# Optimization experiments

Hardware: AMD Instinct MI355X
Metric: run time of the kernel (lower is better)

Reference implementation:

```python
import jax, jax.numpy as jnp
import numpy as np

B, L, N, C = 128, 12, 307, 4
HID = 64
PRE = 3
BN_EPS = 1e-5


def _hamilton(w):
    # w: (in_features//4, out_features) -> hamilton: (in_features, out_features)
    r, i, j, k = jnp.split(w, 4, axis=1)
    return jnp.concatenate([
        jnp.concatenate([r, -i, -j, -k], axis=0),
        jnp.concatenate([i, r, -k, j], axis=0),
        jnp.concatenate([j, k, r, -i], axis=0),
        jnp.concatenate([k, -j, i, r], axis=0),
    ], axis=1)


def setup_inputs() -> dict:
    key = jax.random.key(0)
    ks = jax.random.split(key, 14)

    def u(k, shape, s):
        return jax.random.uniform(k, shape, dtype=jnp.float32, minval=-s, maxval=s)

    history_data = jax.random.uniform(ks[0], (B, L, N, C), dtype=jnp.float32)
    adj = jax.random.uniform(ks[1], (N, N), dtype=jnp.float32)
    # QGNN layer weights (space='q'): layer0 (C//4, HID), layer1 (HID//4, HID)
    w0 = u(ks[2], (C // 4, HID), (6.0 / (C // 4 + HID)) ** 0.5)
    w1 = u(ks[3], (HID // 4, HID), (6.0 / (HID // 4 + HID)) ** 0.5)
    # BatchNorm1d (eval-mode) params for the 2 layers
    bn_gamma = jnp.ones((2, HID), jnp.float32)
    bn_beta = jnp.zeros((2, HID), jnp.float32)
    bn_mean = jnp.zeros((2, HID), jnp.float32)
    bn_var = jnp.ones((2, HID), jnp.float32)
    tid_emb = jax.random.normal(ks[4], (288, 5), dtype=jnp.float32)
    dw_emb = jax.random.normal(ks[5], (7, 5), dtype=jnp.float32)
    gin = HID + 11
    sg = (1.0 / HID) ** 0.5
    w_ih = u(ks[6], (3 * HID, gin), sg)
    w_hh = u(ks[7], (3 * HID, HID), sg)
    b_ih = u(ks[8], (3 * HID,), sg)
    b_hh = u(ks[9], (3 * HID,), sg)
    fc_w = u(ks[10], (1, HID), sg)
    fc_b = u(ks[11], (1,), sg)
    return dict(history_data=history_data, adj=adj, w0=w0, w1=w1,
                bn_gamma=bn_gamma, bn_beta=bn_beta, bn_mean=bn_mean, bn_var=bn_var,
                tid_emb=tid_emb, dw_emb=dw_emb,
                w_ih=w_ih, w_hh=w_hh, b_ih=b_ih, b_hh=b_hh,
                fc_w=fc_w, fc_b=fc_b)


def reference(history_data, adj, w0, w1, bn_gamma, bn_beta, bn_mean, bn_var,
              tid_emb, dw_emb, w_ih, w_hh, b_ih, b_hh, fc_w, fc_b):
    b, l, n, c = history_data.shape
    hist = jnp.transpose(history_data, (0, 2, 1, 3))  # (B, N, L, C)
    speed = hist[..., :1]
    tid = jnp.round(hist[..., 1] * 287).astype(jnp.int32)
    dw = jnp.round(hist[..., 2] * 6).astype(jnp.int32)
    T_D = tid_emb[tid]  # (B, N, L, 5)
    D_W = dw_emb[dw]    # (B, N, L, 5)

    # symmetric adjacency normalization: D^{-1/2} (A + I) D^{-1/2}
    a = adj + jnp.eye(n, dtype=adj.dtype)
    dinv = jnp.sum(a, axis=1) ** -0.5
    a_n = dinv[:, None] * a * dinv[None, :]

    # QGNN layers, vectorized over all timesteps (same weights every t; dropout=identity in eval)
    x = hist
    for i, w in enumerate([w0, w1]):
        ham = _hamilton(w)
        support = jnp.einsum('bnlc,cd->bnld', x, ham)
        out = jnp.einsum('nm,bmld->bnld', a_n, support)
        scale = bn_gamma[i] / jnp.sqrt(bn_var[i] + BN_EPS)
        out = (out - bn_mean[i]) * scale + bn_beta[i]
        x = jnp.tanh(out)

    feat = jnp.concatenate([x, speed, T_D, D_W], axis=-1)  # (B, N, L, HID+11)
    seq = feat.reshape(b * n, l, -1).transpose(1, 0, 2)     # (L, B*N, HID+11)

    hid = w_hh.shape[1]

    def gru_step(h, xt):
        gi = xt @ w_ih.T + b_ih
        gh = h @ w_hh.T + b_hh
        ir, iz, inn = jnp.split(gi, 3, axis=-1)
        hr, hz, hn = jnp.split(gh, 3, axis=-1)
        r = jax.nn.sigmoid(ir + hr)
        z = jax.nn.sigmoid(iz + hz)
        ncand = jnp.tanh(inn + r * hn)
        h_new = (1.0 - z) * ncand + z * h
        return h_new, h_new

    h0 = jnp.zeros((b * n, hid), feat.dtype)
    _, hs = jax.lax.scan(gru_step, h0, seq)        # (L, B*N, HID)
    hs = hs.transpose(1, 0, 2).reshape(b, n, l, hid)
    out = jax.nn.relu(hs[:, :, -PRE:, :])
    out = out @ fc_w.T + fc_b                       # (B, N, PRE, 1)
    return jnp.transpose(out, (0, 2, 1, 3))         # (B, PRE, N, 1)
```

## Files before the change

kernel.cpp:

```cpp
#include <hip/hip_runtime.h>
#include <hip/hip_fp16.h>


#define NND 307
#define BBATCH 128
#define LSEQ 12
#define HIDN 64
#define JTOT (BBATCH*LSEQ*HIDN)
#define NROWS (NND*BBATCH)
#define KPAD 320
#define MSTR 312
#define F2S 80

#define OFF_DINV  0
#define OFF_HAM0  320
#define OFF_HAM1  576
#define OFF_WIHP  4672
#define OFF_WHHP  12352
#define OFF_ANG   18496
#define OFF_S1T   69696
#define OFF_S0T   15405120
#define OFF_FEATH 15405120

typedef _Float16 half8 __attribute__((ext_vector_type(8)));
typedef float f32x4 __attribute__((ext_vector_type(4)));

__global__ void k_dinv(const float* __restrict__ adj, float* __restrict__ dinv){
  int n = blockIdx.x; int lane = threadIdx.x;
  float s = 0.f;
  for (int m = lane; m < NND; m += 64) s += adj[n*NND+m] + (m==n ? 1.f : 0.f);
  #pragma unroll
  for (int o = 32; o > 0; o >>= 1) s += __shfl_down(s, o);
  if (lane == 0) dinv[n] = 1.f/sqrtf(s);
}

__global__ void k_anG(const float* __restrict__ adj, const float* __restrict__ dinv,
                      __half* __restrict__ anG){
  int id = blockIdx.x*256 + threadIdx.x;
  if (id >= KPAD*KPAD) return;
  int n = id / KPAD, m = id % KPAD;
  float v = 0.f;
  if (n < NND && m < NND)
    v = dinv[n] * (adj[n*NND+m] + (n==m ? 1.f : 0.f)) * dinv[m];
  int ks = m >> 5, g = (m >> 3) & 3, j = m & 7;
  anG[(((ks*4 + g)*320 + n) << 3) + j] = __float2half(v);
}

__global__ void k_ham(const float* __restrict__ w0, const float* __restrict__ w1,
                      float* __restrict__ ham0T, float* __restrict__ ham1){
  const int  comp[4][4] = {{0,1,2,3},{1,0,3,2},{2,3,0,1},{3,2,1,0}};
  const float sgn[4][4] = {{1.f,1.f,1.f,1.f},{-1.f,1.f,1.f,-1.f},
                           {-1.f,-1.f,1.f,1.f},{-1.f,1.f,-1.f,1.f}};
  int id = blockIdx.x*256 + threadIdx.x;
  if (id < 64) {
    int d = id, qb = d>>4, cc = d&15;
    #pragma unroll
    for (int c = 0; c < 4; ++c)
      ham0T[d*4+c] = sgn[c][qb] * w0[comp[c][qb]*16 + cc];
  }
  int id1 = id - 256;
  if (id1 >= 0 && id1 < 4096) {
    int drow = id1 >> 6, d = id1 & 63;
    int pb = drow>>4, rr = drow&15, qb = d>>4, cc = d&15;
    ham1[id1] = sgn[pb][qb] * w1[rr*64 + comp[pb][qb]*16 + cc];
  }
}

__global__ void k_wT(const float* __restrict__ w_ih, const float* __restrict__ w_hh,
                     __half* __restrict__ wihP, __half* __restrict__ whhP){
  int id = blockIdx.x*256 + threadIdx.x;
  if (id < 10*192*8) {
    int j = id & 7, col = (id >> 3) % 192, g = id / (192*8);
    int k = g*8 + j;
    wihP[id] = __float2half(k < 75 ? w_ih[col*75 + k] : 0.f);
  } else {
    int id2 = id - 10*192*8;
    if (id2 < 8*192*8) {
      int j = id2 & 7, col = (id2 >> 3) % 192, g = id2 / (192*8);
      whhP[id2] = __float2half(w_hh[col*64 + g*8 + j]);
    }
  }
}

__global__ __launch_bounds__(256) void k_s0(const float* __restrict__ hist,
                                            const float* __restrict__ ham0Tg,
                                            __half* __restrict__ S0T){
  __shared__ float4 histL[320];
  const int t = threadIdx.x;
  const int bl = blockIdx.x;
  for (int k = t; k < 320; k += 256)
    histL[k] = (k < NND) ? *(const float4*)(hist + ((size_t)bl*NND + k)*4)
                         : make_float4(0.f,0.f,0.f,0.f);
  __syncthreads();
  if (t < 154) {
    const int k0 = 2*t;
    const float4 hA = histL[k0], hB = histL[k0+1];
    const size_t jb = (size_t)bl*64;
    for (int d = 0; d < 64; ++d) {
      float4 h0 = *(const float4*)(ham0Tg + d*4);
      float vA = hA.x*h0.x + hA.y*h0.y + hA.z*h0.z + hA.w*h0.w;
      float vB = hB.x*h0.x + hB.y*h0.y + hB.z*h0.z + hB.w*h0.w;
      __half2 p = __floats2half2_rn(vA, vB);
      if (k0 + 1 < NND) *(__half2*)(S0T + (jb + d)*MSTR + k0) = p;
      else              S0T[(jb + d)*MSTR + k0] = __low2half(p);
    }
  }
}

__global__ void k_extras(const float* __restrict__ hist, const float* __restrict__ tid_emb,
                         const float* __restrict__ dw_emb, __half* __restrict__ feat2){
  int id = blockIdx.x*256 + threadIdx.x;
  if (id >= LSEQ*NROWS) return;
  int lq = id / NROWS, row = id % NROWS;
  int n = row >> 7, b = row & 127;
  const float* h = hist + ((size_t)(b*LSEQ + lq)*NND + n)*4;
  union { __half h16[16]; uint4 v[2]; } u;
  u.h16[0] = __float2half(h[0]);
  int ti  = (int)rintf(h[1]*287.f);
  int dwi = (int)rintf(h[2]*6.f);
  #pragma unroll
  for (int c = 0; c < 5; ++c) u.h16[1+c] = __float2half(tid_emb[ti*5+c]);
  #pragma unroll
  for (int c = 0; c < 5; ++c) u.h16[6+c] = __float2half(dw_emb[dwi*5+c]);
  #pragma unroll
  for (int c = 11; c < 16; ++c) u.h16[c] = __float2half(0.f);
  uint4* dst = (uint4*)(feat2 + (size_t)id*F2S + 64);
  dst[0] = u.v[0]; dst[1] = u.v[1];
}

struct SG1 {
  union {
    struct { __half A[2][4][64][8]; __half B[2][4][128][8]; } m;
    struct { float x1[64][132]; } e;
  } u;
  float ham1s[64][64];
  float sc[64], bi[64];
};

__global__ __launch_bounds__(256) void k_gemm1(
    const __half* __restrict__ anG, const __half* __restrict__ S0T,
    const float* __restrict__ ham1g,
    const float* __restrict__ bng, const float* __restrict__ bnb,
    const float* __restrict__ bnm, const float* __restrict__ bnv,
    __half* __restrict__ S1T){
  __shared__ SG1 s;
  const int t = threadIdx.x;
  const int l = t & 63, wv = t >> 6;
  const int xcd = blockIdx.x & 7, idx = blockIdx.x >> 3;
  const int bidj = xcd*96 + idx/5, bidm = idx % 5;
  const int m0 = bidm*64, j0 = bidj*128;
  if (t < 64) {
    float sc = bng[t] / sqrtf(bnv[t] + 1e-5f);
    s.sc[t] = sc; s.bi[t] = bnb[t] - bnm[t]*sc;
  }
  for (int i = t; i < 4096; i += 256) (&s.ham1s[0][0])[i] = ham1g[i];

  const int jB = t >> 1, hB = t & 1;
  const int moff = (wv>>1)*32, joff = (wv&1)*64;

  f32x4 acc[2][4];
  #pragma unroll
  for (int a=0;a<2;++a)
    #pragma unroll
    for (int b=0;b<4;++b) acc[a][b] = (f32x4){0.f,0.f,0.f,0.f};

  {
    uint4 av = *(const uint4*)(anG + (((wv*320) + m0 + l) << 3));
    const __half* bs = S0T + (size_t)(j0 + jB)*MSTR + hB*16;
    uint4 b0 = *(const uint4*)bs;
    uint4 b1 = *(const uint4*)(bs + 8);
    *(uint4*)&s.u.m.A[0][wv][l][0]      = av;
    *(uint4*)&s.u.m.B[0][hB*2][jB][0]   = b0;
    *(uint4*)&s.u.m.B[0][hB*2+1][jB][0] = b1;
  }
  __syncthreads();

  int cur = 0;
  for (int ks = 0; ks < 10; ++ks) {
    uint4 nav, nb0, nb1;
    if (ks < 9) {
      nav = *(const uint4*)(anG + ((((ks+1)*4 + wv)*320 + m0 + l) << 3));
      const __half* bs = S0T + (size_t)(j0 + jB)*MSTR + (ks+1)*32 + hB*16;
      nb0 = *(const uint4*)bs;
      nb1 = *(const uint4*)(bs + 8);
    }
    half8 a8[2], b8[4];
    #pragma unroll
    for (int mf = 0; mf < 2; ++mf)
      a8[mf] = *(const half8*)&s.u.m.A[cur][l>>4][moff + mf*16 + (l&15)][0];
    #pragma unroll
    for (int jf = 0; jf < 4; ++jf)
      b8[jf] = *(const half8*)&s.u.m.B[cur][l>>4][joff + jf*16 + (l&15)][0];
    #pragma unroll
    for (int mf = 0; mf < 2; ++mf)
      #pragma unroll
      for (int jf = 0; jf < 4; ++jf)
        acc[mf][jf] = __builtin_amdgcn_mfma_f32_16x16x32_f16(a8[mf], b8[jf], acc[mf][jf], 0, 0, 0);
    if (ks < 9) {
      *(uint4*)&s.u.m.A[cur^1][wv][l][0]      = nav;
      *(uint4*)&s.u.m.B[cur^1][hB*2][jB][0]   = nb0;
      *(uint4*)&s.u.m.B[cur^1][hB*2+1][jB][0] = nb1;
      __syncthreads();
      cur ^= 1;
    }
  }
  __syncthreads();

  #pragma unroll
  for (int mf = 0; mf < 2; ++mf)
    #pragma unroll
    for (int jf = 0; jf < 4; ++jf)
      #pragma unroll
      for (int r = 0; r < 4; ++r) {
        int mm = moff + mf*16 + (l>>4)*4 + r;
        int jc = joff + jf*16 + (l&15);
        int d = jc & 63;
        s.u.e.x1[mm][jc] = tanhf(acc[mf][jf][r]*s.sc[d] + s.bi[d]);
      }
  __syncthreads();
  const int tx = t & 31, ty = t >> 5;
  const int g64 = (tx >= 16) ? 64 : 0;
  const int dp = (tx & 15)*4;
  float e[8][4];
  #pragma unroll
  for (int r=0;r<8;++r)
    #pragma unroll
    for (int c=0;c<4;++c) e[r][c]=0.f;
  #pragma unroll 4
  for (int dd4 = 0; dd4 < 16; ++dd4) {
    float4 hb0 = *(const float4*)&s.ham1s[dd4*4+0][dp];
    float4 hb1 = *(const float4*)&s.ham1s[dd4*4+1][dp];
    float4 hb2 = *(const float4*)&s.ham1s[dd4*4+2][dp];
    float4 hb3 = *(const float4*)&s.ham1s[dd4*4+3][dp];
    #pragma unroll
    for (int r = 0; r < 8; ++r) {
      float4 xr = *(const float4*)&s.u.e.x1[ty*8+r][g64 + dd4*4];
      e[r][0] = fmaf(xr.x, hb0.x, fmaf(xr.y, hb1.x, fmaf(xr.z, hb2.x, fmaf(xr.w, hb3.x, e[r][0]))));
      e[r][1] = fmaf(xr.x, hb0.y, fmaf(xr.y, hb1.y, fmaf(xr.z, hb2.y, fmaf(xr.w, hb3.y, e[r][1]))));
      e[r][2] = fmaf(xr.x, hb0.z, fmaf(xr.y, hb1.z, fmaf(xr.z, hb2.z, fmaf(xr.w, hb3.z, e[r][2]))));
      e[r][3] = fmaf(xr.x, hb0.w, fmaf(xr.y, hb1.w, fmaf(xr.z, hb2.w, fmaf(xr.w, hb3.w, e[r][3]))));
    }
  }
  const int mbase = m0 + ty*8;
  if (mbase < MSTR) {
    #pragma unroll
    for (int c = 0; c < 4; ++c) {
      union { __half h[8]; uint4 v; } pk;
      #pragma unroll
      for (int r = 0; r < 8; ++r) pk.h[r] = __float2half(e[r][c]);
      int jout = j0 + g64 + dp + c;
      *(uint4*)(S1T + (size_t)jout*MSTR + mbase) = pk.v;
    }
  }
}

struct SG2 {
  union {
    struct { __half A[2][4][64][8]; __half B[2][4][128][8]; } m;
    struct { __half x2[64][2][72]; } e;
  } u;
  float sc[64], bi[64];
};

__global__ __launch_bounds__(256) void k_gemm2(
    const __half* __restrict__ anG, const __half* __restrict__ S1T,
    const float* __restrict__ bng, const float* __restrict__ bnb,
    const float* __restrict__ bnm, const float* __restrict__ bnv,
    __half* __restrict__ feat2){
  __shared__ SG2 s;
  const int t = threadIdx.x;
  const int l = t & 63, wv = t >> 6;
  const int xcd = blockIdx.x & 7, idx = blockIdx.x >> 3;
  const int bidj = xcd*96 + idx/5, bidm = idx % 5;
  const int m0 = bidm*64, j0 = bidj*128;
  if (t < 64) {
    float sc = bng[64+t] / sqrtf(bnv[64+t] + 1e-5f);
    s.sc[t] = sc; s.bi[t] = bnb[64+t] - bnm[64+t]*sc;
  }
  const int jB = t >> 1, hB = t & 1;
  const int moff = (wv>>1)*32, joff = (wv&1)*64;

  f32x4 acc[2][4];
  #pragma unroll
  for (int a=0;a<2;++a)
    #pragma unroll
    for (int b=0;b<4;++b) acc[a][b] = (f32x4){0.f,0.f,0.f,0.f};

  {
    uint4 av = *(const uint4*)(anG + (((wv*320) + m0 + l) << 3));
    const __half* bs = S1T + (size_t)(j0 + jB)*MSTR + hB*16;
    uint4 b0 = *(const uint4*)bs;
    uint4 b1 = *(const uint4*)(bs + 8);
    *(uint4*)&s.u.m.A[0][wv][l][0]      = av;
    *(uint4*)&s.u.m.B[0][hB*2][jB][0]   = b0;
    *(uint4*)&s.u.m.B[0][hB*2+1][jB][0] = b1;
  }
  __syncthreads();

  int cur = 0;
  for (int ks = 0; ks < 10; ++ks) {
    uint4 nav, nb0, nb1;
    if (ks < 9) {
      nav = *(const uint4*)(anG + ((((ks+1)*4 + wv)*320 + m0 + l) << 3));
      const __half* bs = S1T + (size_t)(j0 + jB)*MSTR + (ks+1)*32 + hB*16;
      nb0 = *(const uint4*)bs;
      nb1 = *(const uint4*)(bs + 8);
    }
    half8 a8[2], b8[4];
    #pragma unroll
    for (int mf = 0; mf < 2; ++mf)
      a8[mf] = *(const half8*)&s.u.m.A[cur][l>>4][moff + mf*16 + (l&15)][0];
    #pragma unroll
    for (int jf = 0; jf < 4; ++jf)
      b8[jf] = *(const half8*)&s.u.m.B[cur][l>>4][joff + jf*16 + (l&15)][0];
    #pragma unroll
    for (int mf = 0; mf < 2; ++mf)
      #pragma unroll
      for (int jf = 0; jf < 4; ++jf)
        acc[mf][jf] = __builtin_amdgcn_mfma_f32_16x16x32_f16(a8[mf], b8[jf], acc[mf][jf], 0, 0, 0);
    if (ks < 9) {
      *(uint4*)&s.u.m.A[cur^1][wv][l][0]      = nav;
      *(uint4*)&s.u.m.B[cur^1][hB*2][jB][0]   = nb0;
      *(uint4*)&s.u.m.B[cur^1][hB*2+1][jB][0] = nb1;
      __syncthreads();
      cur ^= 1;
    }
  }
  __syncthreads();
  #pragma unroll
  for (int mf = 0; mf < 2; ++mf)
    #pragma unroll
    for (int jf = 0; jf < 4; ++jf)
      #pragma unroll
      for (int r = 0; r < 4; ++r) {
        int mm = moff + mf*16 + (l>>4)*4 + r;
        int jc = joff + jf*16 + (l&15);
        int bl = jc >> 6, d = jc & 63;
        float v = tanhf(acc[mf][jf][r]*s.sc[d] + s.bi[d]);
        s.u.e.x2[mm][bl][d] = __float2half(v);
      }
  __syncthreads();
  {
    int pr = t >> 1, hf = t & 1;
    int mm = pr >> 1, bl = pr & 1;
    int n = m0 + mm;
    if (n < NND) {
      int jg = j0 + bl*64;
      int b = jg/768, lq = (jg/64)%12;
      __half* dst = feat2 + ((size_t)lq*NROWS + n*BBATCH + b)*F2S + hf*32;
      const __half* srcl = &s.u.e.x2[mm][bl][hf*32];
      #pragma unroll
      for (int i = 0; i < 4; ++i)
        *(uint4*)(dst + i*8) = *(const uint4*)(srcl + i*8);
    }
  }
}

__global__ __launch_bounds__(512, 2) void k_gru(
    const __half* __restrict__ feat2, const __half* __restrict__ wihP,
    const __half* __restrict__ whhP, const float* __restrict__ b_ih,
    const float* __restrict__ b_hh, const float* __restrict__ fc_w,
    const float* __restrict__ fc_b, float* __restrict__ out){
  __shared__ __half wih[10*192*8];
  __shared__ __half whh[8*192*8];
  __shared__ __half xt[10*64*8];
  __shared__ __half Hs[8*64*8];
  __shared__ __half zst[16];
  __shared__ float red[4][2][16];

  const int t = threadIdx.x;
  const int l = t & 63, wv = t >> 6;
  const int mt = wv >> 1, ng = wv & 1;
  const int row0 = blockIdx.x * 64;

  for (int i = t; i < 10*192; i += 512) ((uint4*)wih)[i] = ((const uint4*)wihP)[i];
  for (int i = t; i < 8*192; i += 512)  ((uint4*)whh)[i] = ((const uint4*)whhP)[i];
  for (int i = t; i < 8*64; i += 512)   ((uint4*)Hs)[i] = make_uint4(0,0,0,0);
  if (t < 2) ((uint4*)zst)[t] = make_uint4(0,0,0,0);

  float bR[2], bZ[2], bI[2], bH[2], fw[2];
  #pragma unroll
  for (int s2 = 0; s2 < 2; ++s2) {
    int d = ng*32 + s2*16 + (l & 15);
    bR[s2] = b_ih[d]     + b_hh[d];
    bZ[s2] = b_ih[64+d]  + b_hh[64+d];
    bI[s2] = b_ih[128+d];
    bH[s2] = b_hh[128+d];
    fw[s2] = fc_w[d];
  }
  const float fcb = fc_b[0];
  float hreg[8];
  #pragma unroll
  for (int i = 0; i < 8; ++i) hreg[i] = 0.f;

  const int rst = t >> 3, qst = t & 7;
  {
    const __half* src = feat2 + ((size_t)(row0 + rst))*F2S;
    *(uint4*)&xt[(qst*64 + rst)*8] = *(const uint4*)(src + qst*8);
    if (qst < 2) *(uint4*)&xt[((qst+8)*64 + rst)*8] = *(const uint4*)(src + (qst+8)*8);
  }
  __syncthreads();

  const int rowA = mt*16 + (l & 15);
  const int gq = l >> 4;
  const int colb = l & 15;
  const __half* axt0 = &xt[((0+gq)*64 + rowA)*8];
  const __half* axt1 = &xt[((4+gq)*64 + rowA)*8];
  const __half* axt2 = (gq < 2) ? &xt[((8+gq)*64 + rowA)*8] : zst;
  const __half* ah0  = &Hs[((0+gq)*64 + rowA)*8];
  const __half* ah1  = &Hs[((4+gq)*64 + rowA)*8];
  const __half* bi0  = &wih[((0+gq)*192 + colb)*8];
  const __half* bi1  = &wih[((4+gq)*192 + colb)*8];
  const __half* bi2  = (gq < 2) ? &wih[((8+gq)*192 + colb)*8] : zst;
  const int ntm2 = (gq < 2) ? 128 : 0;
  const __half* bh0  = &whh[((0+gq)*192 + colb)*8];
  const __half* bh1  = &whh[((4+gq)*192 + colb)*8];

  for (int ts = 0; ts < 12; ++ts) {
    half8 agi0 = *(const half8*)axt0;
    half8 agi1 = *(const half8*)axt1;
    half8 agi2 = *(const half8*)axt2;
    half8 agh0 = *(const half8*)ah0;
    half8 agh1 = *(const half8*)ah1;
    f32x4 aR[2], aZ[2], aIn[2], aHn[2];
    #pragma unroll
    for (int s2 = 0; s2 < 2; ++s2) {
      aR[s2] = (f32x4){0.f,0.f,0.f,0.f}; aZ[s2] = (f32x4){0.f,0.f,0.f,0.f};
      aIn[s2] = (f32x4){0.f,0.f,0.f,0.f}; aHn[s2] = (f32x4){0.f,0.f,0.f,0.f};
    }
    #pragma unroll
    for (int s2 = 0; s2 < 2; ++s2) {
      const int ntr = ng*2 + s2, ntz = 4 + ng*2 + s2, ntn = 8 + ng*2 + s2;
      aR[s2] = __builtin_amdgcn_mfma_f32_16x16x32_f16(agi0, *(const half8*)(bi0 + ntr*128), aR[s2], 0,0,0);
      aR[s2] = __builtin_amdgcn_mfma_f32_16x16x32_f16(agi1, *(const half8*)(bi1 + ntr*128), aR[s2], 0,0,0);
      aR[s2] = __builtin_amdgcn_mfma_f32_16x16x32_f16(agi2, *(const half8*)(bi2 + ntr*ntm2), aR[s2], 0,0,0);
      aR[s2] = __builtin_amdgcn_mfma_f32_16x16x32_f16(agh0, *(const half8*)(bh0 + ntr*128), aR[s2], 0,0,0);
      aR[s2] = __builtin_amdgcn_mfma_f32_16x16x32_f16(agh1, *(const half8*)(bh1 + ntr*128), aR[s2], 0,0,0);
      aZ[s2] = __builtin_amdgcn_mfma_f32_16x16x32_f16(agi0, *(const half8*)(bi0 + ntz*128), aZ[s2], 0,0,0);
      aZ[s2] = __builtin_amdgcn_mfma_f32_16x16x32_f16(agi1, *(const half8*)(bi1 + ntz*128), aZ[s2], 0,0,0);
      aZ[s2] = __builtin_amdgcn_mfma_f32_16x16x32_f16(agi2, *(const half8*)(bi2 + ntz*ntm2), aZ[s2], 0,0,0);
      aZ[s2] = __builtin_amdgcn_mfma_f32_16x16x32_f16(agh0, *(const half8*)(bh0 + ntz*128), aZ[s2], 0,0,0);
      aZ[s2] = __builtin_amdgcn_mfma_f32_16x16x32_f16(agh1, *(const half8*)(bh1 + ntz*128), aZ[s2], 0,0,0);
      aIn[s2] = __builtin_amdgcn_mfma_f32_16x16x32_f16(agi0, *(const half8*)(bi0 + ntn*128), aIn[s2], 0,0,0);
      aIn[s2] = __builtin_amdgcn_mfma_f32_16x16x32_f16(agi1, *(const half8*)(bi1 + ntn*128), aIn[s2], 0,0,0);
      aIn[s2] = __builtin_amdgcn_mfma_f32_16x16x32_f16(agi2, *(const half8*)(bi2 + ntn*ntm2), aIn[s2], 0,0,0);
      aHn[s2] = __builtin_amdgcn_mfma_f32_16x16x32_f16(agh0, *(const half8*)(bh0 + ntn*128), aHn[s2], 0,0,0);
      aHn[s2] = __builtin_amdgcn_mfma_f32_16x16x32_f16(agh1, *(const half8*)(bh1 + ntn*128), aHn[s2], 0,0,0);
    }
    float hnew[8];
    #pragma unroll
    for (int s2 = 0; s2 < 2; ++s2)
      #pragma unroll
      for (int rg = 0; rg < 4; ++rg) {
        const int i = s2*4 + rg;
        float pr = aR[s2][rg] + bR[s2];
        float pz = aZ[s2][rg] + bZ[s2];
        float pn = aIn[s2][rg] + bI[s2];
        float ph = aHn[s2][rg] + bH[s2];
        float r = 1.f / (1.f + exp2f(-1.44269504f * pr));
        float z = 1.f / (1.f + exp2f(-1.44269504f * pz));
        float e2 = exp2f(2.88539008f * (pn + r*ph));
        float nc = 1.f - 2.f/(e2 + 1.f);
        hnew[i] = (1.f - z)*nc + z*hreg[i];
        hreg[i] = hnew[i];
      }
    if (ts >= 9) {
      #pragma unroll
      for (int rg = 0; rg < 4; ++rg) {
        float p = fmaxf(hnew[rg],0.f)*fw[0] + fmaxf(hnew[4+rg],0.f)*fw[1];
        p += __shfl_xor(p, 1); p += __shfl_xor(p, 2);
        p += __shfl_xor(p, 4); p += __shfl_xor(p, 8);
        if (colb == 0) red[mt][ng][gq*4 + rg] = p;
      }
    }
    __syncthreads();
    if (ts >= 9 && ng == 0 && colb == 0) {
      #pragma unroll
      for (int rg = 0; rg < 4; ++rg) {
        int rr = gq*4 + rg;
        float sum = red[mt][0][rr] + red[mt][1][rr] + fcb;
        int grow = row0 + mt*16 + rr;
        out[((grow & 127)*3 + (ts-9))*NND + (grow >> 7)] = sum;
      }
    }
    if (ts < 11) {
      #pragma unroll
      for (int s2 = 0; s2 < 2; ++s2) {
        const int d = ng*32 + s2*16 + colb;
        #pragma unroll
        for (int rg = 0; rg < 4; ++rg) {
          int rw = mt*16 + gq*4 + rg;
          Hs[((d>>3)*64 + rw)*8 + (d&7)] = __float2half(hnew[s2*4+rg]);
        }
      }
      const __half* src = feat2 + ((size_t)(ts+1)*NROWS + row0 + rst)*F2S;
      *(uint4*)&xt[(qst*64 + rst)*8] = *(const uint4*)(src + qst*8);
      if (qst < 2) *(uint4*)&xt[((qst+8)*64 + rst)*8] = *(const uint4*)(src + (qst+8)*8);
    }
    __syncthreads();
  }
}

extern "C" void kernel_launch(void* const* d_in, const int* in_sizes, int n_in,
                              void* d_out, int out_size, void* d_ws, size_t ws_size,
                              hipStream_t stream) {
  const float* hist    = (const float*)d_in[0];
  const float* adj     = (const float*)d_in[1];
  const float* w0      = (const float*)d_in[2];
  const float* w1      = (const float*)d_in[3];
  const float* bng     = (const float*)d_in[4];
  const float* bnb     = (const float*)d_in[5];
  const float* bnm     = (const float*)d_in[6];
  const float* bnv     = (const float*)d_in[7];
  const float* tid_emb = (const float*)d_in[8];
  const float* dw_emb  = (const float*)d_in[9];
  const float* w_ih    = (const float*)d_in[10];
  const float* w_hh    = (const float*)d_in[11];
  const float* b_ih    = (const float*)d_in[12];
  const float* b_hh    = (const float*)d_in[13];
  const float* fc_w    = (const float*)d_in[14];
  const float* fc_b    = (const float*)d_in[15];

  float* wsf   = (float*)d_ws;
  float* dinv  = wsf + OFF_DINV;
  float* ham0T = wsf + OFF_HAM0;
  float* ham1  = wsf + OFF_HAM1;
  __half* wihP  = (__half*)(wsf + OFF_WIHP);
  __half* whhP  = (__half*)(wsf + OFF_WHHP);
  __half* anG   = (__half*)(wsf + OFF_ANG);
  __half* S1T   = (__half*)(wsf + OFF_S1T);
  __half* S0T   = (__half*)(wsf + OFF_S0T);
  __half* feat2 = (__half*)(wsf + OFF_FEATH);
  float* outp  = (float*)d_out;

  k_dinv  <<<NND, 64, 0, stream>>>(adj, dinv);
  k_anG   <<<(KPAD*KPAD + 255)/256, 256, 0, stream>>>(adj, dinv, anG);
  k_ham   <<<17, 256, 0, stream>>>(w0, w1, ham0T, ham1);
  k_wT    <<<108, 256, 0, stream>>>(w_ih, w_hh, wihP, whhP);
  k_s0    <<<BBATCH*LSEQ, 256, 0, stream>>>(hist, ham0T, S0T);
  k_gemm1 <<<5*768, 256, 0, stream>>>(anG, S0T, ham1, bng, bnb, bnm, bnv, S1T);
  k_extras<<<(LSEQ*NROWS + 255)/256, 256, 0, stream>>>(hist, tid_emb, dw_emb, feat2);
  k_gemm2 <<<5*768, 256, 0, stream>>>(anG, S1T, bng, bnb, bnm, bnv, feat2);
  k_gru   <<<NROWS/64, 512, 0, stream>>>(feat2, wihP, whhP, b_ih, b_hh, fc_w, fc_b, outp);
}
```

Baseline: 405.5 us.

## Compute gemm1 epilogue Hamilton projection with fp16 MFMA and fast tanh

The second-layer Hamilton weight multiply in k_gemm1's epilogue is moved from fp32 scalar FMAs over shared memory onto 16x16x32 fp16 MFMA. The weights are pre-packed into an MFMA-friendly half layout, and the tanh output is staged in half precision. Output is transposed through shared memory for coalesced stores, and tanhf is replaced by an exp2-based approximation in both GEMM kernels. The aim is to cut epilogue ALU work and shared-memory footprint, in exchange for lower precision in the intermediate and in tanh.

```diff
diff --git a/kernel.cpp b/kernel.cpp
--- a/kernel.cpp
+++ b/kernel.cpp
@@ -14,7 +14,7 @@
 
 #define OFF_DINV  0
 #define OFF_HAM0  320
-#define OFF_HAM1  576
+#define OFF_HAM1B 576
 #define OFF_WIHP  4672
 #define OFF_WHHP  12352
 #define OFF_ANG   18496
@@ -24,6 +24,11 @@
 
 typedef _Float16 half8 __attribute__((ext_vector_type(8)));
 typedef float f32x4 __attribute__((ext_vector_type(4)));
+
+__device__ __forceinline__ float tanh_fast(float v){
+  float e2 = exp2f(2.88539008f * v);
+  return 1.f - 2.f/(e2 + 1.f);
+}
 
 __global__ void k_dinv(const float* __restrict__ adj, float* __restrict__ dinv){
   int n = blockIdx.x; int lane = threadIdx.x;
@@ -47,7 +52,7 @@
 }
 
 __global__ void k_ham(const float* __restrict__ w0, const float* __restrict__ w1,
-                      float* __restrict__ ham0T, float* __restrict__ ham1){
+                      float* __restrict__ ham0T, __half* __restrict__ ham1B){
   const int  comp[4][4] = {{0,1,2,3},{1,0,3,2},{2,3,0,1},{3,2,1,0}};
   const float sgn[4][4] = {{1.f,1.f,1.f,1.f},{-1.f,1.f,1.f,-1.f},
                            {-1.f,-1.f,1.f,1.f},{-1.f,1.f,-1.f,1.f}};
@@ -60,9 +65,10 @@
   }
   int id1 = id - 256;
   if (id1 >= 0 && id1 < 4096) {
-    int drow = id1 >> 6, d = id1 & 63;
-    int pb = drow>>4, rr = drow&15, qb = d>>4, cc = d&15;
-    ham1[id1] = sgn[pb][qb] * w1[rr*64 + comp[pb][qb]*16 + cc];
+    int din = id1 >> 6, d = id1 & 63;
+    int pb = din>>4, rr = din&15, qb = d>>4, cc = d&15;
+    float val = sgn[pb][qb] * w1[rr*64 + comp[pb][qb]*16 + cc];
+    ham1B[(((din>>3)*64) + d)*8 + (din&7)] = __float2half(val);
   }
 }
 
@@ -131,15 +137,14 @@
 struct SG1 {
   union {
     struct { __half A[2][4][64][8]; __half B[2][4][128][8]; } m;
-    struct { float x1[64][132]; } e;
+    struct { __half xh[2][8][64][8]; __half h1b[8][64][8]; __half s1l[128][72]; } e;
   } u;
-  float ham1s[64][64];
   float sc[64], bi[64];
 };
 
 __global__ __launch_bounds__(256) void k_gemm1(
     const __half* __restrict__ anG, const __half* __restrict__ S0T,
-    const float* __restrict__ ham1g,
+    const __half* __restrict__ ham1Bg,
     const float* __restrict__ bng, const float* __restrict__ bnb,
     const float* __restrict__ bnm, const float* __restrict__ bnv,
     __half* __restrict__ S1T){
@@ -153,7 +158,6 @@
     float sc = bng[t] / sqrtf(bnv[t] + 1e-5f);
     s.sc[t] = sc; s.bi[t] = bnb[t] - bnm[t]*sc;
   }
-  for (int i = t; i < 4096; i += 256) (&s.ham1s[0][0])[i] = ham1g[i];
 
   const int jB = t >> 1, hB = t & 1;
   const int moff = (wv>>1)*32, joff = (wv&1)*64;
@@ -206,6 +210,12 @@
   }
   __syncthreads();
 
+  {
+    const uint4* srcg = (const uint4*)ham1Bg;
+    uint4* dstg = (uint4*)&s.u.e.h1b[0][0][0];
+    #pragma unroll
+    for (int i = 0; i < 2; ++i) dstg[t + i*256] = srcg[t + i*256];
+  }
   #pragma unroll
   for (int mf = 0; mf < 2; ++mf)
     #pragma unroll
@@ -215,42 +225,50 @@
         int mm = moff + mf*16 + (l>>4)*4 + r;
         int jc = joff + jf*16 + (l&15);
         int d = jc & 63;
-        s.u.e.x1[mm][jc] = tanhf(acc[mf][jf][r]*s.sc[d] + s.bi[d]);
-      }
-  __syncthreads();
-  const int tx = t & 31, ty = t >> 5;
-  const int g64 = (tx >= 16) ? 64 : 0;
-  const int dp = (tx & 15)*4;
-  float e[8][4];
-  #pragma unroll
-  for (int r=0;r<8;++r)
-    #pragma unroll
-    for (int c=0;c<4;++c) e[r][c]=0.f;
-  #pragma unroll 4
-  for (int dd4 = 0; dd4 < 16; ++dd4) {
-    float4 hb0 = *(const float4*)&s.ham1s[dd4*4+0][dp];
-    float4 hb1 = *(const float4*)&s.ham1s[dd4*4+1][dp];
-    float4 hb2 = *(const float4*)&s.ham1s[dd4*4+2][dp];
-    float4 hb3 = *(const float4*)&s.ham1s[dd4*4+3][dp];
-    #pragma unroll
-    for (int r = 0; r < 8; ++r) {
-      float4 xr = *(const float4*)&s.u.e.x1[ty*8+r][g64 + dd4*4];
-      e[r][0] = fmaf(xr.x, hb0.x, fmaf(xr.y, hb1.x, fmaf(xr.z, hb2.x, fmaf(xr.w, hb3.x, e[r][0]))));
-      e[r][1] = fmaf(xr.x, hb0.y, fmaf(xr.y, hb1.y, fmaf(xr.z, hb2.y, fmaf(xr.w, hb3.y, e[r][1]))));
-      e[r][2] = fmaf(xr.x, hb0.z, fmaf(xr.y, hb1.z, fmaf(xr.z, hb2.z, fmaf(xr.w, hb3.z, e[r][2]))));
-      e[r][3] = fmaf(xr.x, hb0.w, fmaf(xr.y, hb1.w, fmaf(xr.z, hb2.w, fmaf(xr.w, hb3.w, e[r][3]))));
-    }
-  }
-  const int mbase = m0 + ty*8;
-  if (mbase < MSTR) {
-    #pragma unroll
-    for (int c = 0; c < 4; ++c) {
-      union { __half h[8]; uint4 v; } pk;
-      #pragma unroll
-      for (int r = 0; r < 8; ++r) pk.h[r] = __float2half(e[r][c]);
-      int jout = j0 + g64 + dp + c;
-      *(uint4*)(S1T + (size_t)jout*MSTR + mbase) = pk.v;
-    }
+        float v = tanh_fast(acc[mf][jf][r]*s.sc[d] + s.bi[d]);
+        s.u.e.xh[jc>>6][d>>3][mm][d&7] = __float2half(v);
+      }
+  __syncthreads();
+  f32x4 acc2[2][4];
+  #pragma unroll
+  for (int a=0;a<2;++a)
+    #pragma unroll
+    for (int b=0;b<4;++b) acc2[a][b] = (f32x4){0.f,0.f,0.f,0.f};
+  const int gq = l >> 4, cb = l & 15;
+  const int blw = wv & 1;
+  #pragma unroll
+  for (int ks2 = 0; ks2 < 2; ++ks2) {
+    half8 a2[2];
+    #pragma unroll
+    for (int mf = 0; mf < 2; ++mf)
+      a2[mf] = *(const half8*)&s.u.e.xh[blw][ks2*4+gq][moff + mf*16 + cb][0];
+    #pragma unroll
+    for (int jf = 0; jf < 4; ++jf) {
+      half8 b2 = *(const half8*)&s.u.e.h1b[ks2*4+gq][jf*16 + cb][0];
+      #pragma unroll
+      for (int mf = 0; mf < 2; ++mf)
+        acc2[mf][jf] = __builtin_amdgcn_mfma_f32_16x16x32_f16(a2[mf], b2, acc2[mf][jf], 0, 0, 0);
+    }
+  }
+  #pragma unroll
+  for (int mf = 0; mf < 2; ++mf)
+    #pragma unroll
+    for (int jf = 0; jf < 4; ++jf)
+      #pragma unroll
+      for (int r = 0; r < 4; ++r) {
+        int node = moff + mf*16 + gq*4 + r;
+        int ro = blw*64 + jf*16 + cb;
+        s.u.e.s1l[ro][node] = __float2half(acc2[mf][jf][r]);
+      }
+  __syncthreads();
+  {
+    int jj = t >> 1, hf = t & 1;
+    __half* dst = S1T + (size_t)(j0 + jj)*MSTR + m0 + hf*32;
+    const __half* srcl = &s.u.e.s1l[jj][hf*32];
+    #pragma unroll
+    for (int i = 0; i < 4; ++i)
+      if (m0 + hf*32 + i*8 < MSTR)
+        *(uint4*)(dst + i*8) = *(const uint4*)(srcl + i*8);
   }
 }
 
@@ -336,7 +354,7 @@
         int mm = moff + mf*16 + (l>>4)*4 + r;
         int jc = joff + jf*16 + (l&15);
         int bl = jc >> 6, d = jc & 63;
-        float v = tanhf(acc[mf][jf][r]*s.sc[d] + s.bi[d]);
+        float v = tanh_fast(acc[mf][jf][r]*s.sc[d] + s.bi[d]);
         s.u.e.x2[mm][bl][d] = __float2half(v);
       }
   __syncthreads();
@@ -524,7 +542,7 @@
   float* wsf   = (float*)d_ws;
   float* dinv  = wsf + OFF_DINV;
   float* ham0T = wsf + OFF_HAM0;
-  float* ham1  = wsf + OFF_HAM1;
+  __half* ham1B = (__half*)(wsf + OFF_HAM1B);
   __half* wihP  = (__half*)(wsf + OFF_WIHP);
   __half* whhP  = (__half*)(wsf + OFF_WHHP);
   __half* anG   = (__half*)(wsf + OFF_ANG);
@@ -535,10 +553,10 @@
 
   k_dinv  <<<NND, 64, 0, stream>>>(adj, dinv);
   k_anG   <<<(KPAD*KPAD + 255)/256, 256, 0, stream>>>(adj, dinv, anG);
-  k_ham   <<<17, 256, 0, stream>>>(w0, w1, ham0T, ham1);
+  k_ham   <<<17, 256, 0, stream>>>(w0, w1, ham0T, ham1B);
   k_wT    <<<108, 256, 0, stream>>>(w_ih, w_hh, wihP, whhP);
   k_s0    <<<BBATCH*LSEQ, 256, 0, stream>>>(hist, ham0T, S0T);
-  k_gemm1 <<<5*768, 256, 0, stream>>>(anG, S0T, ham1, bng, bnb, bnm, bnv, S1T);
+  k_gemm1 <<<5*768, 256, 0, stream>>>(anG, S0T, ham1B, bng, bnb, bnm, bnv, S1T);
   k_extras<<<(LSEQ*NROWS + 255)/256, 256, 0, stream>>>(hist, tid_emb, dw_emb, feat2);
   k_gemm2 <<<5*768, 256, 0, stream>>>(anG, S1T, bng, bnb, bnm, bnv, feat2);
   k_gru   <<<NROWS/64, 512, 0, stream>>>(feat2, wihP, whhP, b_ih, b_hh, fc_w, fc_b, outp);
```

After: 333.5 us. 1.22x faster.
